# Kernel tuning notes

Hardware: AMD Instinct MI355X
Metric: run time of the kernel (lower is better)

The kernel has to match this reference:

```python
import math
import jax, jax.numpy as jnp
import numpy as np

D, H, L, DFF, V = 512, 8, 6, 2048, 32000
B, S = 2, 2048
PAD = 1


def _layernorm(x, g, b, eps=1e-5):
    m = x.mean(-1, keepdims=True)
    v = ((x - m) ** 2).mean(-1, keepdims=True)
    return (x - m) / jnp.sqrt(v + eps) * g + b


def _mha(qx, kx, w, b, mask, h=H):
    # w: [4, D, D] (q,k,v,out), b: [4, D]; mask broadcastable to [B,1,Sq,Sk]
    bs, sq, d = qx.shape
    dk = d // h
    def proj(x, i):
        return (x @ w[i] + b[i]).reshape(bs, -1, h, dk).transpose(0, 2, 1, 3)
    q, k, v = proj(qx, 0), proj(kx, 1), proj(kx, 2)
    scores = jnp.einsum('bhqd,bhkd->bhqk', q, k) / math.sqrt(dk)
    scores = jnp.where(mask, scores, -jnp.inf)
    attn = jax.nn.softmax(scores, axis=-1)
    out = jnp.einsum('bhqk,bhkd->bhqd', attn, v).transpose(0, 2, 1, 3).reshape(bs, sq, d)
    return out @ w[3] + b[3]


def _ff(x, w1, b1, w2, b2):
    return jax.nn.relu(x @ w1 + b1) @ w2 + b2


def _sinusoidal_pe(max_len, d):
    pos = np.arange(max_len)[:, None].astype(np.float64)
    div = np.exp(np.arange(0, d, 2) * (-math.log(10000.0) / d))
    pe = np.zeros((max_len, d), np.float32)
    pe[:, 0::2] = np.sin(pos * div)
    pe[:, 1::2] = np.cos(pos * div)
    return jnp.asarray(pe[None])  # [1, max_len, d]


def setup_inputs() -> dict:
    key = jax.random.key(0)
    ks = iter(jax.random.split(key, 32))
    def w(shape):
        return jax.random.normal(next(ks), shape, jnp.float32) * 0.02
    inp = {
        'src': jax.random.randint(next(ks), (B, S), 2, V),
        'tgt': jax.random.randint(next(ks), (B, S), 2, V),
        'src_emb': w((V, D)),
        'tgt_emb': w((V, D)),
        'pe': _sinusoidal_pe(S, D),
        'enc_attn_w': w((L, 4, D, D)), 'enc_attn_b': jnp.zeros((L, 4, D)),
        'enc_ff_w1': w((L, D, DFF)), 'enc_ff_b1': jnp.zeros((L, DFF)),
        'enc_ff_w2': w((L, DFF, D)), 'enc_ff_b2': jnp.zeros((L, D)),
        'enc_ln_g': jnp.ones((L, 2, D)), 'enc_ln_b': jnp.zeros((L, 2, D)),
        'dec_self_w': w((L, 4, D, D)), 'dec_self_b': jnp.zeros((L, 4, D)),
        'dec_src_w': w((L, 4, D, D)), 'dec_src_b': jnp.zeros((L, 4, D)),
        'dec_ff_w1': w((L, D, DFF)), 'dec_ff_b1': jnp.zeros((L, DFF)),
        'dec_ff_w2': w((L, DFF, D)), 'dec_ff_b2': jnp.zeros((L, D)),
        'dec_ln_g': jnp.ones((L, 3, D)), 'dec_ln_b': jnp.zeros((L, 3, D)),
        'ln_g': jnp.ones((D,)), 'ln_b': jnp.zeros((D,)),
        'fc_w': w((D, V)), 'fc_b': jnp.zeros((V,)),
    }
    return inp


def reference(src, tgt, src_emb, tgt_emb, pe,
              enc_attn_w, enc_attn_b, enc_ff_w1, enc_ff_b1, enc_ff_w2, enc_ff_b2,
              enc_ln_g, enc_ln_b,
              dec_self_w, dec_self_b, dec_src_w, dec_src_b,
              dec_ff_w1, dec_ff_b1, dec_ff_w2, dec_ff_b2, dec_ln_g, dec_ln_b,
              ln_g, ln_b, fc_w, fc_b):
    s_len, t_len = src.shape[1], tgt.shape[1]
    src_mask = (src != PAD)[:, None, None, :]                      # [B,1,1,Ss]
    tril = jnp.tril(jnp.ones((t_len, t_len), bool))
    tgt_mask = (tgt != PAD)[:, None, None, :] & tril[None, None]   # [B,1,St,St]

    x = src_emb[src] + pe[:, :s_len]
    for l in range(L):
        x2 = _layernorm(x, enc_ln_g[l, 0], enc_ln_b[l, 0])
        x = x + _mha(x2, x2, enc_attn_w[l], enc_attn_b[l], src_mask)
        x2 = _layernorm(x, enc_ln_g[l, 1], enc_ln_b[l, 1])
        x = x + _ff(x2, enc_ff_w1[l], enc_ff_b1[l], enc_ff_w2[l], enc_ff_b2[l])
    memory = x

    y = tgt_emb[tgt] + pe[:, :t_len]
    for l in range(L):
        y2 = _layernorm(y, dec_ln_g[l, 0], dec_ln_b[l, 0])
        y = y + _mha(y2, y2, dec_self_w[l], dec_self_b[l], tgt_mask)
        y2 = _layernorm(y, dec_ln_g[l, 1], dec_ln_b[l, 1])
        y = y + _mha(y2, memory, dec_src_w[l], dec_src_b[l], src_mask)
        y2 = _layernorm(y, dec_ln_g[l, 2], dec_ln_b[l, 2])
        y = y + _ff(y2, dec_ff_w1[l], dec_ff_b1[l], dec_ff_w2[l], dec_ff_b2[l])

    return _layernorm(y, ln_g, ln_b) @ fc_w + fc_b  # [B, St, V]
```

## Files before the change

### kernel.cpp

```cpp
#include <hip/hip_runtime.h>
#include <math.h>

#define D_MODEL 512
#define NHEAD   8
#define NLAYER  6
#define DFF_    2048
#define VOCAB   32000
#define BATCH   2
#define SEQ     2048
#define NTOK    (BATCH*SEQ)
#define PAD_ID  1

typedef __attribute__((ext_vector_type(8))) short s16x8;
typedef __attribute__((ext_vector_type(4))) float f32x4;
typedef unsigned short u16;
typedef unsigned int   u32;
typedef unsigned long long u64;

__device__ __forceinline__ u16 f2bf(float x) {
  u32 u = __builtin_bit_cast(u32, x);
  u += 0x7FFFu + ((u >> 16) & 1u);
  return (u16)(u >> 16);
}

__device__ __forceinline__ float exp2i(float x) {
  float r; asm("v_exp_f32 %0, %1" : "=v"(r) : "v"(x)); return r;
}

__device__ __forceinline__ void gload16(const void* g, void* l) {
  __builtin_amdgcn_global_load_lds(
      (const __attribute__((address_space(1))) u32*)g,
      (__attribute__((address_space(3))) u32*)l, 16, 0, 0);
}

#define CEXP 0.1803368802f

__global__ __launch_bounds__(256) void embed2_kernel(
    const int* __restrict__ src, const int* __restrict__ tgt,
    const float* __restrict__ se, const float* __restrict__ te,
    const float* __restrict__ pe, float* __restrict__ xe, float* __restrict__ yd)
{
  const int z = blockIdx.y;
  const int* tok = z ? tgt : src;
  const float* emb = z ? te : se;
  float* out = z ? yd : xe;
  const int total = NTOK * D_MODEL;
  for (int i = blockIdx.x * 256 + threadIdx.x; i < total; i += gridDim.x * 256) {
    int t = i >> 9;
    int d = i & 511;
    int s = t & (SEQ - 1);
    out[i] = emb[(size_t)tok[t] * D_MODEL + d] + pe[(size_t)s * D_MODEL + d];
  }
}

__global__ __launch_bounds__(64) void padmask2_kernel(
    const int* __restrict__ src, const int* __restrict__ tgt,
    u64* __restrict__ pmS, u64* __restrict__ pmT)
{
  const int z = blockIdx.z;
  const int* tok = z ? tgt : src;
  u64* pm = z ? pmT : pmS;
  int b = blockIdx.y, t = blockIdx.x;
  int lane = threadIdx.x;
  u64 m = __ballot(tok[(size_t)b * SEQ + t * 64 + lane] != PAD_ID);
  if (lane == 0) pm[b * (SEQ / 64) + t] = m;
}

__global__ __launch_bounds__(256) void ln_kernel(
    const float* __restrict__ x, const float* __restrict__ g,
    const float* __restrict__ bb, u16* __restrict__ y)
{
  const int lane = threadIdx.x & 63;
  const size_t row = (size_t)blockIdx.x * 4 + (threadIdx.x >> 6);
  const float* xr = x + row * D_MODEL + lane * 8;
  float4 v0 = *(const float4*)xr;
  float4 v1 = *(const float4*)(xr + 4);
  float sum = (v0.x + v0.y) + (v0.z + v0.w) + (v1.x + v1.y) + (v1.z + v1.w);
  float ss = v0.x * v0.x + v0.y * v0.y + v0.z * v0.z + v0.w * v0.w
           + v1.x * v1.x + v1.y * v1.y + v1.z * v1.z + v1.w * v1.w;
  #pragma unroll
  for (int o = 1; o < 64; o <<= 1) {
    sum += __shfl_xor(sum, o, 64);
    ss  += __shfl_xor(ss, o, 64);
  }
  float mean = sum * (1.0f / D_MODEL);
  float inv = rsqrtf(ss * (1.0f / D_MODEL) - mean * mean + 1e-5f);
  float4 g0 = *(const float4*)&g[lane * 8];
  float4 g1 = *(const float4*)&g[lane * 8 + 4];
  float4 c0 = *(const float4*)&bb[lane * 8];
  float4 c1 = *(const float4*)&bb[lane * 8 + 4];
  uint4 o;
  o.x = (u32)f2bf((v0.x - mean) * inv * g0.x + c0.x) | ((u32)f2bf((v0.y - mean) * inv * g0.y + c0.y) << 16);
  o.y = (u32)f2bf((v0.z - mean) * inv * g0.z + c0.z) | ((u32)f2bf((v0.w - mean) * inv * g0.w + c0.w) << 16);
  o.z = (u32)f2bf((v1.x - mean) * inv * g1.x + c1.x) | ((u32)f2bf((v1.y - mean) * inv * g1.y + c1.y) << 16);
  o.w = (u32)f2bf((v1.z - mean) * inv * g1.z + c1.z) | ((u32)f2bf((v1.w - mean) * inv * g1.w + c1.w) << 16);
  *(uint4*)&y[row * D_MODEL + lane * 8] = o;
}

__global__ __launch_bounds__(256) void tconv2_kernel(
    const float* __restrict__ s0, const float* __restrict__ s1,
    u16* __restrict__ d0, u16* __restrict__ d1, int zsplit, int K, int N)
{
  __shared__ float tile[64][65];
  const int z = blockIdx.z;
  const float* src = (z < zsplit) ? s0 + (size_t)z * K * N : s1 + (size_t)(z - zsplit) * K * N;
  u16* dst = (z < zsplit) ? d0 + (size_t)z * K * N : d1 + (size_t)(z - zsplit) * K * N;
  const int n0 = blockIdx.x * 64, k0 = blockIdx.y * 64;
  const int t = threadIdx.x;
  const int cr = t >> 4, cc = (t & 15) * 4;
  #pragma unroll
  for (int it = 0; it < 4; ++it) {
    int kr = cr + it * 16;
    float4 v = *(const float4*)&src[(size_t)(k0 + kr) * N + n0 + cc];
    tile[kr][cc] = v.x; tile[kr][cc + 1] = v.y; tile[kr][cc + 2] = v.z; tile[kr][cc + 3] = v.w;
  }
  __syncthreads();
  #pragma unroll
  for (int it = 0; it < 4; ++it) {
    int nr = cr + it * 16;
    u32 lo = (u32)f2bf(tile[cc + 0][nr]) | ((u32)f2bf(tile[cc + 1][nr]) << 16);
    u32 hi = (u32)f2bf(tile[cc + 2][nr]) | ((u32)f2bf(tile[cc + 3][nr]) << 16);
    uint2 pk; pk.x = lo; pk.y = hi;
    *(uint2*)&dst[(size_t)(n0 + nr) * K + k0 + cc] = pk;
  }
}

__global__ __launch_bounds__(256) void tconv3_kernel(
    const float* __restrict__ s0, const float* __restrict__ s1,
    const float* __restrict__ s2, u16* __restrict__ dst0)
{
  __shared__ float tile[64][65];
  const int z = blockIdx.z;
  const float* src = (z < 24) ? s0 + (size_t)z * 262144
                   : (z < 48) ? s1 + (size_t)(z - 24) * 262144
                              : s2 + (size_t)(z - 48) * 262144;
  u16* dst = dst0 + (size_t)z * 262144;
  const int n0 = blockIdx.x * 64, k0 = blockIdx.y * 64;
  const int t = threadIdx.x;
  const int cr = t >> 4, cc = (t & 15) * 4;
  #pragma unroll
  for (int it = 0; it < 4; ++it) {
    int kr = cr + it * 16;
    float4 v = *(const float4*)&src[(size_t)(k0 + kr) * 512 + n0 + cc];
    tile[kr][cc] = v.x; tile[kr][cc + 1] = v.y; tile[kr][cc + 2] = v.z; tile[kr][cc + 3] = v.w;
  }
  __syncthreads();
  #pragma unroll
  for (int it = 0; it < 4; ++it) {
    int nr = cr + it * 16;
    u32 lo = (u32)f2bf(tile[cc + 0][nr]) | ((u32)f2bf(tile[cc + 1][nr]) << 16);
    u32 hi = (u32)f2bf(tile[cc + 2][nr]) | ((u32)f2bf(tile[cc + 3][nr]) << 16);
    uint2 pk; pk.x = lo; pk.y = hi;
    *(uint2*)&dst[(size_t)(n0 + nr) * 512 + k0 + cc] = pk;
  }
}

template<int MODE, int BM, int BN, int MAP>
__global__ __launch_bounds__(256, 2) void mm_kernel(
    const u16* __restrict__ A, const u16* __restrict__ Wt,
    const float* __restrict__ bias, const float* __restrict__ res,
    void* __restrict__ Cout, u16* __restrict__ vtOut,
    int M, int N, int K,
    long long wStride, long long bStride, long long cStride)
{
  constexpr int MI = BM / 32;
  constexpr int NI = BN / 32;
  constexpr bool DB = (BM == 64 && BN == 64);
  __shared__ u16 sh[(DB ? 2 : 1) * (BM + BN) * 64];
  const int z = blockIdx.z;
  size_t wOff, bOff;
  if (MAP == 1) {
    wOff = (size_t)(z >> 1) * 4 * 262144 + (size_t)(1 + (z & 1)) * 262144;
    bOff = (size_t)(z >> 1) * 4 * 512 + (size_t)(1 + (z & 1)) * 512;
  } else {
    wOff = (size_t)z * wStride;
    bOff = (size_t)z * bStride;
  }
  Wt += wOff;
  bias += bOff;
  const int bm = blockIdx.y * BM, bn = blockIdx.x * BN;
  const int tid = threadIdx.x, lane = tid & 63, w = tid >> 6;
  const int wm = w >> 1, wn = w & 1;
  const int l15 = lane & 15, l4 = lane >> 4;
  const int wrow0 = wm * (BM / 2), wcol0 = wn * (BN / 2);
  const u16* aBase = A  + (size_t)bm * K;
  const u16* bBase = Wt + (size_t)bn * K;
  f32x4 acc[MI][NI] = {};

  auto mfma_step = [&](const u16* Asb, const u16* Bsb) {
    #pragma unroll
    for (int ks = 0; ks < 2; ++ks) {
      s16x8 af[MI], bf[NI];
      #pragma unroll
      for (int mi = 0; mi < MI; ++mi) {
        int rr = wrow0 + mi * 16 + l15;
        af[mi] = *(const s16x8*)&Asb[(rr << 6) + (((ks * 4 + l4) ^ (rr & 7)) << 3)];
      }
      #pragma unroll
      for (int ni = 0; ni < NI; ++ni) {
        int rr = wcol0 + ni * 16 + l15;
        bf[ni] = *(const s16x8*)&Bsb[(rr << 6) + (((ks * 4 + l4) ^ (rr & 7)) << 3)];
      }
      #pragma unroll
      for (int mi = 0; mi < MI; ++mi)
        #pragma unroll
        for (int ni = 0; ni < NI; ++ni)
          acc[mi][ni] = __builtin_amdgcn_mfma_f32_16x16x32_bf16(af[mi], bf[ni], acc[mi][ni], 0, 0, 0);
    }
  };

  if constexpr (DB) {
    u16* As0 = sh;
    u16* As1 = sh + 64 * 64;
    u16* Bs0 = sh + 2 * 64 * 64;
    u16* Bs1 = sh + 3 * 64 * 64;
    auto stage = [&](int k0, u16* Ad, u16* Bd) {
      #pragma unroll
      for (int i = 0; i < 2; ++i) {
        int lin = i * 256 + tid;
        int r = lin >> 3, sp = lin & 7;
        gload16(aBase + (size_t)r * K + k0 + ((sp ^ (r & 7)) * 8), &Ad[(i * 256 + w * 64) * 8]);
      }
      #pragma unroll
      for (int i = 0; i < 2; ++i) {
        int lin = i * 256 + tid;
        int r = lin >> 3, sp = lin & 7;
        gload16(bBase + (size_t)r * K + k0 + ((sp ^ (r & 7)) * 8), &Bd[(i * 256 + w * 64) * 8]);
      }
    };
    stage(0, As0, Bs0);
    __syncthreads();
    const int nt = K >> 6;
    for (int t = 0; t < nt; ++t) {
      const bool even = !(t & 1);
      u16* Ac = even ? As0 : As1;
      u16* Bc = even ? Bs0 : Bs1;
      if (t + 1 < nt) stage((t + 1) << 6, even ? As1 : As0, even ? Bs1 : Bs0);
      mfma_step(Ac, Bc);
      __syncthreads();
    }
  } else {
    u16* As = sh;
    u16* Bs = sh + BM * 64;
    for (int k0 = 0; k0 < K; k0 += 64) {
      #pragma unroll
      for (int i = 0; i < BM / 32; ++i) {
        int lin = i * 256 + tid;
        int r = lin >> 3, sp = lin & 7;
        gload16(aBase + (size_t)r * K + k0 + ((sp ^ (r & 7)) * 8), &As[(i * 256 + w * 64) * 8]);
      }
      #pragma unroll
      for (int i = 0; i < BN / 32; ++i) {
        int lin = i * 256 + tid;
        int r = lin >> 3, sp = lin & 7;
        gload16(bBase + (size_t)r * K + k0 + ((sp ^ (r & 7)) * 8), &Bs[(i * 256 + w * 64) * 8]);
      }
      __syncthreads();
      mfma_step(As, Bs);
      __syncthreads();
    }
  }

  const bool vpath = (MODE == 4 && z == 2) || (MODE == 5 && (z & 1) == 1);
  if (vpath) {
    u16* TT = sh;
    #pragma unroll
    for (int mi = 0; mi < MI; ++mi)
      #pragma unroll
      for (int ni = 0; ni < NI; ++ni)
        #pragma unroll
        for (int r = 0; r < 4; ++r) {
          int rowl = wrow0 + mi * 16 + l4 * 4 + r;
          int coll = wcol0 + ni * 16 + l15;
          TT[coll * 72 + rowl] = f2bf(acc[mi][ni][r] + bias[bn + coll]);
        }
    __syncthreads();
    const int b = bm >> 11, s0loc = bm & 2047, h = bn >> 6;
    const int layer = (MODE == 5) ? (z >> 1) : 0;
    u16* vbase = vtOut + (size_t)layer * ((size_t)NTOK * D_MODEL)
               + ((size_t)(b * NHEAD + h) * 64) * SEQ;
    int d = tid >> 2, sc = (tid & 3) * 16;
    s16x8 v0 = *(const s16x8*)&TT[d * 72 + sc];
    s16x8 v1 = *(const s16x8*)&TT[d * 72 + sc + 8];
    *(s16x8*)(vbase + (size_t)d * SEQ + s0loc + sc) = v0;
    *(s16x8*)(vbase + (size_t)d * SEQ + s0loc + sc + 8) = v1;
    return;
  }

  const int zi = (MAP == 1) ? (z >> 1) : z;
  #pragma unroll
  for (int ni = 0; ni < NI; ++ni) {
    int col = bn + wcol0 + ni * 16 + l15;
    float bb = bias[col];
    #pragma unroll
    for (int mi = 0; mi < MI; ++mi) {
      #pragma unroll
      for (int r = 0; r < 4; ++r) {
        int row = bm + wrow0 + mi * 16 + l4 * 4 + r;
        size_t off = (size_t)zi * cStride + (size_t)row * N + col;
        float v = acc[mi][ni][r] + bb;
        if (MODE == 1 || MODE == 6) v += res[(size_t)row * N + col];
        if (MODE == 3) v = fmaxf(v, 0.0f);
        if (MODE <= 1 || MODE == 6) ((float*)Cout)[off] = v;
        else                        ((u16*)Cout)[off] = f2bf(v);
        if (MODE == 6) vtOut[(size_t)row * N + col] = f2bf(v);
      }
    }
  }
}

template<int CAUSAL, int QPROJ>
__global__ __launch_bounds__(256, 2) void fattn_kernel(
    const u16* __restrict__ Qg, const u16* __restrict__ Kg,
    const u16* __restrict__ Vt, const u16* __restrict__ Wq,
    const float* __restrict__ qbias, const u64* __restrict__ padm,
    u16* __restrict__ Og)
{
  __shared__ u16 Ks[2][128 * 64];
  __shared__ u16 Vs[2][64 * 128];
  __shared__ u16 Ps[4][16 * 128];
  const int qtile = CAUSAL ? (int)(gridDim.x - 1 - blockIdx.x) : (int)blockIdx.x;
  const int qt = qtile * 64;
  const int h = blockIdx.y, b = blockIdx.z;
  const int tid = threadIdx.x, lane = tid & 63, w = tid >> 6;
  const int l15 = lane & 15, l4 = lane >> 4;
  const int hoff = h * 64;
  const u16* Kbase = Kg + (size_t)(b * SEQ) * D_MODEL + hoff;
  const u16* Vbase = Vt + (size_t)(b * NHEAD + h) * 64 * SEQ;
  const u64* pmb = padm + b * (SEQ / 64);
  const int qg = qt + w * 16 + l15;

  s16x8 aq[2];
  if constexpr (QPROJ) {
    const u16* xBase = Qg + (size_t)(b * SEQ + qt) * D_MODEL;
    const u16* wBase = Wq + (size_t)hoff * D_MODEL;
    u16* Xs = Ks[0];
    u16* Wsh = Ks[0] + 64 * 64;
    f32x4 qa[4] = {};
    for (int k0 = 0; k0 < 512; k0 += 64) {
      #pragma unroll
      for (int i = 0; i < 2; ++i) {
        int lin = i * 256 + tid;
        int r = lin >> 3, sp = lin & 7;
        gload16(xBase + (size_t)r * D_MODEL + k0 + ((sp ^ (r & 7)) * 8), &Xs[(i * 256 + w * 64) * 8]);
      }
      #pragma unroll
      for (int i = 0; i < 2; ++i) {
        int lin = i * 256 + tid;
        int r = lin >> 3, sp = lin & 7;
        gload16(wBase + (size_t)r * D_MODEL + k0 + ((sp ^ (r & 7)) * 8), &Wsh[(i * 256 + w * 64) * 8]);
      }
      __syncthreads();
      #pragma unroll
      for (int ks = 0; ks < 2; ++ks) {
        int rr = w * 16 + l15;
        s16x8 xa = *(const s16x8*)&Xs[(rr << 6) + (((ks * 4 + l4) ^ (rr & 7)) << 3)];
        #pragma unroll
        for (int ni = 0; ni < 4; ++ni) {
          int rw = ni * 16 + l15;
          s16x8 wb = *(const s16x8*)&Wsh[(rw << 6) + (((ks * 4 + l4) ^ (rw & 7)) << 3)];
          qa[ni] = __builtin_amdgcn_mfma_f32_16x16x32_bf16(xa, wb, qa[ni], 0, 0, 0);
        }
      }
      __syncthreads();
    }
    u16* Qsh = (u16*)Ps;
    #pragma unroll
    for (int ni = 0; ni < 4; ++ni) {
      int col = ni * 16 + l15;
      float bb = qbias[hoff + col];
      #pragma unroll
      for (int r = 0; r < 4; ++r) {
        int row = w * 16 + l4 * 4 + r;
        Qsh[(row << 6) + ((((col >> 3)) ^ (row & 7)) << 3) + (col & 7)] = f2bf(qa[ni][r] + bb);
      }
    }
    __syncthreads();
    {
      int rr = w * 16 + l15;
      aq[0] = *(const s16x8*)&Qsh[(rr << 6) + (((0 + l4) ^ (rr & 7)) << 3)];
      aq[1] = *(const s16x8*)&Qsh[(rr << 6) + (((4 + l4) ^ (rr & 7)) << 3)];
    }
  } else {
    const u16* qp = Qg + (size_t)(b * SEQ + qg) * D_MODEL + hoff + l4 * 8;
    aq[0] = *(const s16x8*)qp;
    aq[1] = *(const s16x8*)(qp + 32);
  }

  f32x4 oacc[4] = {};
  float mrow = -1e30f, lrow = 0.f;
  const int nt = CAUSAL ? (qt >> 7) + 1 : SEQ / 128;

  #define STAGE(KV0, BUF)                                                              \
    {                                                                                  \
      _Pragma("unroll")                                                                \
      for (int it = 0; it < 4; ++it) {                                                 \
        int lin = it * 256 + tid;                                                      \
        int rr = lin >> 3, sp = lin & 7;                                               \
        gload16(Kbase + (size_t)((KV0) + rr) * D_MODEL + ((sp ^ (rr & 7)) * 8),        \
                &Ks[BUF][(it * 256 + w * 64) * 8]);                                    \
      }                                                                                \
      _Pragma("unroll")                                                                \
      for (int it = 0; it < 4; ++it) {                                                 \
        int lin = it * 256 + tid;                                                      \
        int rr = lin >> 4, ko = lin & 15;                                              \
        gload16(Vbase + (size_t)rr * SEQ + (KV0) + ((ko ^ (rr & 15)) * 8),             \
                &Vs[BUF][(it * 256 + w * 64) * 8]);                                    \
      }                                                                                \
    }

  if constexpr (QPROJ) __syncthreads();
  STAGE(0, 0);
  __syncthreads();

  for (int kt = 0; kt < nt; ++kt) {
    const int kv0 = kt * 128;
    const int cur = kt & 1;
    if (kt + 1 < nt) STAGE(kv0 + 128, cur ^ 1);

    f32x4 sac[8] = {};
    #pragma unroll
    for (int ks = 0; ks < 2; ++ks)
      #pragma unroll
      for (int jn = 0; jn < 8; ++jn) {
        int rr = jn * 16 + l15;
        s16x8 ak = *(const s16x8*)&Ks[cur][(rr << 6) + (((ks * 4 + l4) ^ (rr & 7)) << 3)];
        sac[jn] = __builtin_amdgcn_mfma_f32_16x16x32_bf16(ak, aq[ks], sac[jn], 0, 0, 0);
      }

    const u64 m0 = pmb[(kv0 >> 6)];
    const u64 m1 = pmb[(kv0 >> 6) + 1];
    const bool lastC = CAUSAL && (kt == nt - 1);
    if (((m0 & m1) != ~0ull) || lastC) {
      #pragma unroll
      for (int jn = 0; jn < 8; ++jn) {
        u64 mm = (jn < 4) ? m0 : m1;
        #pragma unroll
        for (int r = 0; r < 4; ++r) {
          int kl = (jn & 3) * 16 + l4 * 4 + r;
          int kvg = kv0 + jn * 16 + l4 * 4 + r;
          bool ok = ((mm >> kl) & 1) && (!CAUSAL || kvg <= qg);
          if (!ok) sac[jn][r] = -1e30f;
        }
      }
    }

    float m = sac[0][0];
    #pragma unroll
    for (int jn = 0; jn < 8; ++jn)
      #pragma unroll
      for (int r = 0; r < 4; ++r) m = fmaxf(m, sac[jn][r]);
    m = fmaxf(m, __shfl_xor(m, 16, 64));
    m = fmaxf(m, __shfl_xor(m, 32, 64));

    if (__any(m - mrow > 64.0f)) {
      float mn = fmaxf(mrow, m);
      float sc = exp2i((mrow - mn) * CEXP);
      mrow = mn;
      lrow *= sc;
      #pragma unroll
      for (int jn = 0; jn < 4; ++jn)
        #pragma unroll
        for (int r = 0; r < 4; ++r) oacc[jn][r] *= sc;
    }

    float rs = 0.f;
    #pragma unroll
    for (int jn = 0; jn < 8; ++jn) {
      float p0 = exp2i((sac[jn][0] - mrow) * CEXP);
      float p1 = exp2i((sac[jn][1] - mrow) * CEXP);
      float p2 = exp2i((sac[jn][2] - mrow) * CEXP);
      float p3 = exp2i((sac[jn][3] - mrow) * CEXP);
      rs += (p0 + p1) + (p2 + p3);
      uint2 pk;
      pk.x = (u32)f2bf(p0) | ((u32)f2bf(p1) << 16);
      pk.y = (u32)f2bf(p2) | ((u32)f2bf(p3) << 16);
      int pu = (jn * 4 + l4) ^ ((l15 & 7) << 2);
      *(uint2*)&Ps[w][l15 * 128 + pu * 4] = pk;
    }
    rs += __shfl_xor(rs, 16, 64);
    rs += __shfl_xor(rs, 32, 64);
    lrow += rs;

    #pragma unroll
    for (int ks2 = 0; ks2 < 4; ++ks2) {
      int pu = (ks2 * 8 + l4 * 2) ^ ((l15 & 7) << 2);
      s16x8 pb = *(const s16x8*)&Ps[w][l15 * 128 + pu * 4];
      #pragma unroll
      for (int jn = 0; jn < 4; ++jn) {
        int rr = jn * 16 + l15;
        s16x8 av = *(const s16x8*)&Vs[cur][(rr << 7) + (((ks2 * 4 + l4) ^ (rr & 15)) << 3)];
        oacc[jn] = __builtin_amdgcn_mfma_f32_16x16x32_bf16(av, pb, oacc[jn], 0, 0, 0);
      }
    }
    __syncthreads();
  }
  #undef STAGE

  const float inv = 1.0f / lrow;
  u16* orow = Og + (size_t)(b * SEQ + qg) * D_MODEL + hoff;
  #pragma unroll
  for (int jn = 0; jn < 4; ++jn) {
    uint2 pk;
    pk.x = (u32)f2bf(oacc[jn][0] * inv) | ((u32)f2bf(oacc[jn][1] * inv) << 16);
    pk.y = (u32)f2bf(oacc[jn][2] * inv) | ((u32)f2bf(oacc[jn][3] * inv) << 16);
    *(uint2*)(orow + jn * 16 + l4 * 4) = pk;
  }
}

extern "C" void kernel_launch(void* const* d_in, const int* in_sizes, int n_in,
                              void* d_out, int out_size, void* d_ws, size_t ws_size,
                              hipStream_t stream)
{
  const int*   src        = (const int*)  d_in[0];
  const int*   tgt        = (const int*)  d_in[1];
  const float* src_emb    = (const float*)d_in[2];
  const float* tgt_emb    = (const float*)d_in[3];
  const float* pe         = (const float*)d_in[4];
  const float* enc_attn_w = (const float*)d_in[5];
  const float* enc_attn_b = (const float*)d_in[6];
  const float* enc_ff_w1  = (const float*)d_in[7];
  const float* enc_ff_b1  = (const float*)d_in[8];
  const float* enc_ff_w2  = (const float*)d_in[9];
  const float* enc_ff_b2  = (const float*)d_in[10];
  const float* enc_ln_g   = (const float*)d_in[11];
  const float* enc_ln_bb  = (const float*)d_in[12];
  const float* dec_self_w = (const float*)d_in[13];
  const float* dec_self_b = (const float*)d_in[14];
  const float* dec_src_w  = (const float*)d_in[15];
  const float* dec_src_b  = (const float*)d_in[16];
  const float* dec_ff_w1  = (const float*)d_in[17];
  const float* dec_ff_b1  = (const float*)d_in[18];
  const float* dec_ff_w2  = (const float*)d_in[19];
  const float* dec_ff_b2  = (const float*)d_in[20];
  const float* dec_ln_g   = (const float*)d_in[21];
  const float* dec_ln_bb  = (const float*)d_in[22];
  const float* fin_ln_g   = (const float*)d_in[23];
  const float* fin_ln_b   = (const float*)d_in[24];
  const float* fc_w       = (const float*)d_in[25];
  const float* fc_b       = (const float*)d_in[26];
  float* out = (float*)d_out;

  const size_t DD = (size_t)D_MODEL * D_MODEL;
  const size_t FD = (size_t)D_MODEL * DFF_;
  const size_t TD = (size_t)NTOK * D_MODEL;

  char* ob = (char*)d_out;
  size_t off = 0;
  auto alloco = [&](size_t bytes) { void* p = ob + off; off += (bytes + 255) & ~(size_t)255; return p; };
  u16* wt_enc_attn = (u16*)alloco(24 * DD * 2);
  u16* wt_dec_self = (u16*)alloco(24 * DD * 2);
  u16* wt_dec_src  = (u16*)alloco(24 * DD * 2);
  u16* wt_enc_ff1  = (u16*)alloco(6 * FD * 2);
  u16* wt_enc_ff2  = (u16*)alloco(6 * FD * 2);
  u16* wt_dec_ff1  = (u16*)alloco(6 * FD * 2);
  u16* wt_dec_ff2  = (u16*)alloco(6 * FD * 2);
  u16* qb   = (u16*)alloco(2 * TD * 2);
  u16* kb   = qb + TD;
  u16* vtb  = (u16*)alloco(TD * 2);
  u16* aob  = (u16*)alloco(TD * 2);
  u16* hbb  = (u16*)alloco((size_t)NTOK * DFF_ * 2);
  u16* memb = (u16*)alloco(TD * 2);
  u16* ckb  = (u16*)alloco(6 * TD * 2);
  u16* cvtb = (u16*)alloco(6 * TD * 2);

  char* wsb = (char*)d_ws;
  u16*   fcwt = (u16*)wsb;
  size_t wo = ((size_t)VOCAB * D_MODEL * 2 + 255) & ~(size_t)255;
  float* xe  = (float*)(wsb + wo); wo += TD * 4;
  float* yd  = (float*)(wsb + wo); wo += TD * 4;
  u16*   x2b = (u16*)(wsb + wo);   wo += TD * 2;
  u64*   pmS = (u64*)(wsb + wo);   wo += 1024;
  u64*   pmT = (u64*)(wsb + wo);

  dim3 blk(256);
  dim3 gN512(8, 64, 1), gQKV(8, 64, 3), gCKV(8, 64, 12);
  dim3 gFF1(16, 32, 1), gFC(125, 32, 1);
  dim3 gAttn(SEQ / 64, NHEAD, BATCH);
  dim3 gLN(NTOK / 4);
  const long long llDD = (long long)DD, llTD = (long long)TD;

  padmask2_kernel<<<dim3(SEQ / 64, BATCH, 2), dim3(64), 0, stream>>>(src, tgt, pmS, pmT);
  tconv3_kernel<<<dim3(8, 8, 72), blk, 0, stream>>>(enc_attn_w, dec_self_w, dec_src_w, wt_enc_attn);
  tconv2_kernel<<<dim3(32, 8, 12), blk, 0, stream>>>(enc_ff_w1, dec_ff_w1, wt_enc_ff1, wt_dec_ff1, 6, 512, 2048);
  tconv2_kernel<<<dim3(8, 32, 12), blk, 0, stream>>>(enc_ff_w2, dec_ff_w2, wt_enc_ff2, wt_dec_ff2, 6, 2048, 512);
  tconv2_kernel<<<dim3(500, 8, 1), blk, 0, stream>>>(fc_w, fc_w, fcwt, fcwt, 1, 512, VOCAB);
  embed2_kernel<<<dim3(2048, 2), blk, 0, stream>>>(src, tgt, src_emb, tgt_emb, pe, xe, yd);

  for (int l = 0; l < NLAYER; ++l) {
    ln_kernel<<<gLN, blk, 0, stream>>>(xe, enc_ln_g + (size_t)(l * 2 + 0) * D_MODEL,
                                       enc_ln_bb + (size_t)(l * 2 + 0) * D_MODEL, x2b);
    mm_kernel<4, 64, 64, 0><<<gQKV, blk, 0, stream>>>(x2b, wt_enc_attn + (size_t)l * 4 * DD,
        enc_attn_b + (size_t)l * 4 * D_MODEL, nullptr, qb, vtb, NTOK, 512, 512, llDD, D_MODEL, llTD);
    fattn_kernel<0, 0><<<gAttn, blk, 0, stream>>>(qb, kb, vtb, nullptr, nullptr, pmS, aob);
    mm_kernel<1, 64, 64, 0><<<gN512, blk, 0, stream>>>(aob, wt_enc_attn + (size_t)(l * 4 + 3) * DD,
        enc_attn_b + (size_t)(l * 4 + 3) * D_MODEL, xe, xe, nullptr, NTOK, 512, 512, 0, 0, 0);
    ln_kernel<<<gLN, blk, 0, stream>>>(xe, enc_ln_g + (size_t)(l * 2 + 1) * D_MODEL,
                                       enc_ln_bb + (size_t)(l * 2 + 1) * D_MODEL, x2b);
    mm_kernel<3, 128, 128, 0><<<gFF1, blk, 0, stream>>>(x2b, wt_enc_ff1 + (size_t)l * FD,
        enc_ff_b1 + (size_t)l * DFF_, nullptr, hbb, nullptr, NTOK, DFF_, 512, 0, 0, 0);
    if (l == NLAYER - 1)
      mm_kernel<6, 64, 64, 0><<<gN512, blk, 0, stream>>>(hbb, wt_enc_ff2 + (size_t)l * FD,
          enc_ff_b2 + (size_t)l * D_MODEL, xe, xe, memb, NTOK, 512, DFF_, 0, 0, 0);
    else
      mm_kernel<1, 64, 64, 0><<<gN512, blk, 0, stream>>>(hbb, wt_enc_ff2 + (size_t)l * FD,
          enc_ff_b2 + (size_t)l * D_MODEL, xe, xe, nullptr, NTOK, 512, DFF_, 0, 0, 0);
  }

  mm_kernel<5, 64, 64, 1><<<gCKV, blk, 0, stream>>>(memb, wt_dec_src, dec_src_b, nullptr,
      ckb, cvtb, NTOK, 512, 512, 0, 0, llTD);

  for (int l = 0; l < NLAYER; ++l) {
    const u16* Ws = wt_dec_self + (size_t)l * 4 * DD;
    const u16* Wc = wt_dec_src + (size_t)l * 4 * DD;
    const float* bs  = dec_self_b + (size_t)l * 4 * D_MODEL;
    const float* bcb = dec_src_b + (size_t)l * 4 * D_MODEL;
    ln_kernel<<<gLN, blk, 0, stream>>>(yd, dec_ln_g + (size_t)(l * 3 + 0) * D_MODEL,
                                       dec_ln_bb + (size_t)(l * 3 + 0) * D_MODEL, x2b);
    mm_kernel<4, 64, 64, 0><<<gQKV, blk, 0, stream>>>(x2b, Ws, bs, nullptr, qb, vtb,
                                                      NTOK, 512, 512, llDD, D_MODEL, llTD);
    fattn_kernel<1, 0><<<gAttn, blk, 0, stream>>>(qb, kb, vtb, nullptr, nullptr, pmT, aob);
    mm_kernel<1, 64, 64, 0><<<gN512, blk, 0, stream>>>(aob, Ws + 3 * DD, bs + 3 * D_MODEL, yd, yd,
                                                       nullptr, NTOK, 512, 512, 0, 0, 0);
    ln_kernel<<<gLN, blk, 0, stream>>>(yd, dec_ln_g + (size_t)(l * 3 + 1) * D_MODEL,
                                       dec_ln_bb + (size_t)(l * 3 + 1) * D_MODEL, x2b);
    fattn_kernel<0, 1><<<gAttn, blk, 0, stream>>>(x2b, ckb + (size_t)l * TD, cvtb + (size_t)l * TD,
                                                  Wc, bcb, pmS, aob);
    mm_kernel<1, 64, 64, 0><<<gN512, blk, 0, stream>>>(aob, Wc + 3 * DD, bcb + 3 * D_MODEL, yd, yd,
                                                       nullptr, NTOK, 512, 512, 0, 0, 0);
    ln_kernel<<<gLN, blk, 0, stream>>>(yd, dec_ln_g + (size_t)(l * 3 + 2) * D_MODEL,
                                       dec_ln_bb + (size_t)(l * 3 + 2) * D_MODEL, x2b);
    mm_kernel<3, 128, 128, 0><<<gFF1, blk, 0, stream>>>(x2b, wt_dec_ff1 + (size_t)l * FD,
        dec_ff_b1 + (size_t)l * DFF_, nullptr, hbb, nullptr, NTOK, DFF_, 512, 0, 0, 0);
    mm_kernel<1, 64, 64, 0><<<gN512, blk, 0, stream>>>(hbb, wt_dec_ff2 + (size_t)l * FD,
        dec_ff_b2 + (size_t)l * D_MODEL, yd, yd, nullptr, NTOK, 512, DFF_, 0, 0, 0);
  }

  ln_kernel<<<gLN, blk, 0, stream>>>(yd, fin_ln_g, fin_ln_b, x2b);
  mm_kernel<0, 128, 256, 0><<<gFC, blk, 0, stream>>>(x2b, fcwt, fc_b, nullptr, out, nullptr,
                                                     NTOK, VOCAB, 512, 0, 0, 0);

  (void)in_sizes; (void)n_in; (void)out_size; (void)ws_size;
}
```

Measured before the change: 2.285 ms.

## Shrink attention KV tile to 64, double-buffer square GEMM tiles, swap FC grid order

The flash-attention kernel now processes 64-key tiles instead of 128. This cuts shared memory and register use so launch bounds can ask for 4 blocks per SM, at the cost of twice as many loop iterations and barriers. The GEMM kernel's double-buffered path now covers any square tile size, so the 128x128 FF1 GEMM gets double buffering, which doubles its shared memory. The vocab projection grid is transposed so consecutive blocks walk the M dimension and share the same weight tile, aiming for better L2 reuse of the weights.

```diff
diff --git a/kernel.cpp b/kernel.cpp
--- a/kernel.cpp
+++ b/kernel.cpp
@@ -155,7 +155,7 @@
   }
 }
 
-template<int MODE, int BM, int BN, int MAP>
+template<int MODE, int BM, int BN, int MAP, int XSWAP = 0>
 __global__ __launch_bounds__(256, 2) void mm_kernel(
     const u16* __restrict__ A, const u16* __restrict__ Wt,
     const float* __restrict__ bias, const float* __restrict__ res,
@@ -165,7 +165,7 @@
 {
   constexpr int MI = BM / 32;
   constexpr int NI = BN / 32;
-  constexpr bool DB = (BM == 64 && BN == 64);
+  constexpr bool DB = (BM == BN);
   __shared__ u16 sh[(DB ? 2 : 1) * (BM + BN) * 64];
   const int z = blockIdx.z;
   size_t wOff, bOff;
@@ -178,7 +178,8 @@
   }
   Wt += wOff;
   bias += bOff;
-  const int bm = blockIdx.y * BM, bn = blockIdx.x * BN;
+  const int bm = (XSWAP ? blockIdx.x : blockIdx.y) * BM;
+  const int bn = (XSWAP ? blockIdx.y : blockIdx.x) * BN;
   const int tid = threadIdx.x, lane = tid & 63, w = tid >> 6;
   const int wm = w >> 1, wn = w & 1;
   const int l15 = lane & 15, l4 = lane >> 4;
@@ -211,18 +212,18 @@
 
   if constexpr (DB) {
     u16* As0 = sh;
-    u16* As1 = sh + 64 * 64;
-    u16* Bs0 = sh + 2 * 64 * 64;
-    u16* Bs1 = sh + 3 * 64 * 64;
+    u16* As1 = sh + BM * 64;
+    u16* Bs0 = sh + 2 * BM * 64;
+    u16* Bs1 = sh + 2 * BM * 64 + BN * 64;
     auto stage = [&](int k0, u16* Ad, u16* Bd) {
       #pragma unroll
-      for (int i = 0; i < 2; ++i) {
+      for (int i = 0; i < BM / 32; ++i) {
         int lin = i * 256 + tid;
         int r = lin >> 3, sp = lin & 7;
         gload16(aBase + (size_t)r * K + k0 + ((sp ^ (r & 7)) * 8), &Ad[(i * 256 + w * 64) * 8]);
       }
       #pragma unroll
-      for (int i = 0; i < 2; ++i) {
+      for (int i = 0; i < BN / 32; ++i) {
         int lin = i * 256 + tid;
         int r = lin >> 3, sp = lin & 7;
         gload16(bBase + (size_t)r * K + k0 + ((sp ^ (r & 7)) * 8), &Bd[(i * 256 + w * 64) * 8]);
@@ -310,15 +311,15 @@
 }
 
 template<int CAUSAL, int QPROJ>
-__global__ __launch_bounds__(256, 2) void fattn_kernel(
+__global__ __launch_bounds__(256, 4) void fattn_kernel(
     const u16* __restrict__ Qg, const u16* __restrict__ Kg,
     const u16* __restrict__ Vt, const u16* __restrict__ Wq,
     const float* __restrict__ qbias, const u64* __restrict__ padm,
     u16* __restrict__ Og)
 {
-  __shared__ u16 Ks[2][128 * 64];
-  __shared__ u16 Vs[2][64 * 128];
-  __shared__ u16 Ps[4][16 * 128];
+  __shared__ u16 Ks[2][64 * 64];
+  __shared__ u16 Vs[2][64 * 64];
+  __shared__ u16 Ps[4][16 * 64];
   const int qtile = CAUSAL ? (int)(gridDim.x - 1 - blockIdx.x) : (int)blockIdx.x;
   const int qt = qtile * 64;
   const int h = blockIdx.y, b = blockIdx.z;
@@ -334,8 +335,8 @@
   if constexpr (QPROJ) {
     const u16* xBase = Qg + (size_t)(b * SEQ + qt) * D_MODEL;
     const u16* wBase = Wq + (size_t)hoff * D_MODEL;
-    u16* Xs = Ks[0];
-    u16* Wsh = Ks[0] + 64 * 64;
+    u16* Xs  = Ks[0];
+    u16* Wsh = Vs[0];
     f32x4 qa[4] = {};
     for (int k0 = 0; k0 < 512; k0 += 64) {
       #pragma unroll
@@ -389,22 +390,22 @@
 
   f32x4 oacc[4] = {};
   float mrow = -1e30f, lrow = 0.f;
-  const int nt = CAUSAL ? (qt >> 7) + 1 : SEQ / 128;
+  const int nt = CAUSAL ? (qt >> 6) + 1 : SEQ / 64;
 
   #define STAGE(KV0, BUF)                                                              \
     {                                                                                  \
       _Pragma("unroll")                                                                \
-      for (int it = 0; it < 4; ++it) {                                                 \
+      for (int it = 0; it < 2; ++it) {                                                 \
         int lin = it * 256 + tid;                                                      \
         int rr = lin >> 3, sp = lin & 7;                                               \
         gload16(Kbase + (size_t)((KV0) + rr) * D_MODEL + ((sp ^ (rr & 7)) * 8),        \
                 &Ks[BUF][(it * 256 + w * 64) * 8]);                                    \
       }                                                                                \
       _Pragma("unroll")                                                                \
-      for (int it = 0; it < 4; ++it) {                                                 \
+      for (int it = 0; it < 2; ++it) {                                                 \
         int lin = it * 256 + tid;                                                      \
-        int rr = lin >> 4, ko = lin & 15;                                              \
-        gload16(Vbase + (size_t)rr * SEQ + (KV0) + ((ko ^ (rr & 15)) * 8),             \
+        int rr = lin >> 3, ko = lin & 7;                                               \
+        gload16(Vbase + (size_t)rr * SEQ + (KV0) + ((ko ^ (rr & 7)) * 8),              \
                 &Vs[BUF][(it * 256 + w * 64) * 8]);                                    \
       }                                                                                \
     }
@@ -414,32 +415,30 @@
   __syncthreads();
 
   for (int kt = 0; kt < nt; ++kt) {
-    const int kv0 = kt * 128;
+    const int kv0 = kt * 64;
     const int cur = kt & 1;
-    if (kt + 1 < nt) STAGE(kv0 + 128, cur ^ 1);
-
-    f32x4 sac[8] = {};
+    if (kt + 1 < nt) STAGE(kv0 + 64, cur ^ 1);
+
+    f32x4 sac[4] = {};
     #pragma unroll
     for (int ks = 0; ks < 2; ++ks)
       #pragma unroll
-      for (int jn = 0; jn < 8; ++jn) {
+      for (int jn = 0; jn < 4; ++jn) {
         int rr = jn * 16 + l15;
         s16x8 ak = *(const s16x8*)&Ks[cur][(rr << 6) + (((ks * 4 + l4) ^ (rr & 7)) << 3)];
         sac[jn] = __builtin_amdgcn_mfma_f32_16x16x32_bf16(ak, aq[ks], sac[jn], 0, 0, 0);
       }
 
-    const u64 m0 = pmb[(kv0 >> 6)];
-    const u64 m1 = pmb[(kv0 >> 6) + 1];
+    const u64 m0 = pmb[kv0 >> 6];
     const bool lastC = CAUSAL && (kt == nt - 1);
-    if (((m0 & m1) != ~0ull) || lastC) {
-      #pragma unroll
-      for (int jn = 0; jn < 8; ++jn) {
-        u64 mm = (jn < 4) ? m0 : m1;
+    if ((m0 != ~0ull) || lastC) {
+      #pragma unroll
+      for (int jn = 0; jn < 4; ++jn) {
         #pragma unroll
         for (int r = 0; r < 4; ++r) {
-          int kl = (jn & 3) * 16 + l4 * 4 + r;
-          int kvg = kv0 + jn * 16 + l4 * 4 + r;
-          bool ok = ((mm >> kl) & 1) && (!CAUSAL || kvg <= qg);
+          int kl = jn * 16 + l4 * 4 + r;
+          int kvg = kv0 + kl;
+          bool ok = ((m0 >> kl) & 1) && (!CAUSAL || kvg <= qg);
           if (!ok) sac[jn][r] = -1e30f;
         }
       }
@@ -447,7 +446,7 @@
 
     float m = sac[0][0];
     #pragma unroll
-    for (int jn = 0; jn < 8; ++jn)
+    for (int jn = 0; jn < 4; ++jn)
       #pragma unroll
       for (int r = 0; r < 4; ++r) m = fmaxf(m, sac[jn][r]);
     m = fmaxf(m, __shfl_xor(m, 16, 64));
@@ -466,7 +465,7 @@
 
     float rs = 0.f;
     #pragma unroll
-    for (int jn = 0; jn < 8; ++jn) {
+    for (int jn = 0; jn < 4; ++jn) {
       float p0 = exp2i((sac[jn][0] - mrow) * CEXP);
       float p1 = exp2i((sac[jn][1] - mrow) * CEXP);
       float p2 = exp2i((sac[jn][2] - mrow) * CEXP);
@@ -475,21 +474,21 @@
       uint2 pk;
       pk.x = (u32)f2bf(p0) | ((u32)f2bf(p1) << 16);
       pk.y = (u32)f2bf(p2) | ((u32)f2bf(p3) << 16);
-      int pu = (jn * 4 + l4) ^ ((l15 & 7) << 2);
-      *(uint2*)&Ps[w][l15 * 128 + pu * 4] = pk;
+      int u = (jn * 4 + l4) ^ ((l15 & 7) << 1);
+      *(uint2*)&Ps[w][l15 * 64 + u * 4] = pk;
     }
     rs += __shfl_xor(rs, 16, 64);
     rs += __shfl_xor(rs, 32, 64);
     lrow += rs;
 
     #pragma unroll
-    for (int ks2 = 0; ks2 < 4; ++ks2) {
-      int pu = (ks2 * 8 + l4 * 2) ^ ((l15 & 7) << 2);
-      s16x8 pb = *(const s16x8*)&Ps[w][l15 * 128 + pu * 4];
+    for (int ks2 = 0; ks2 < 2; ++ks2) {
+      int up = (ks2 * 8 + l4 * 2) ^ ((l15 & 7) << 1);
+      s16x8 pb = *(const s16x8*)&Ps[w][l15 * 64 + up * 4];
       #pragma unroll
       for (int jn = 0; jn < 4; ++jn) {
         int rr = jn * 16 + l15;
-        s16x8 av = *(const s16x8*)&Vs[cur][(rr << 7) + (((ks2 * 4 + l4) ^ (rr & 15)) << 3)];
+        s16x8 av = *(const s16x8*)&Vs[cur][(rr << 6) + (((ks2 * 4 + l4) ^ (rr & 7)) << 3)];
         oacc[jn] = __builtin_amdgcn_mfma_f32_16x16x32_bf16(av, pb, oacc[jn], 0, 0, 0);
       }
     }
@@ -575,7 +574,7 @@
 
   dim3 blk(256);
   dim3 gN512(8, 64, 1), gQKV(8, 64, 3), gCKV(8, 64, 12);
-  dim3 gFF1(16, 32, 1), gFC(125, 32, 1);
+  dim3 gFF1(16, 32, 1), gFC(32, 125, 1);
   dim3 gAttn(SEQ / 64, NHEAD, BATCH);
   dim3 gLN(NTOK / 4);
   const long long llDD = (long long)DD, llTD = (long long)TD;
@@ -637,8 +636,8 @@
   }
 
   ln_kernel<<<gLN, blk, 0, stream>>>(yd, fin_ln_g, fin_ln_b, x2b);
-  mm_kernel<0, 128, 256, 0><<<gFC, blk, 0, stream>>>(x2b, fcwt, fc_b, nullptr, out, nullptr,
-                                                     NTOK, VOCAB, 512, 0, 0, 0);
+  mm_kernel<0, 128, 256, 0, 1><<<gFC, blk, 0, stream>>>(x2b, fcwt, fc_b, nullptr, out, nullptr,
+                                                        NTOK, VOCAB, 512, 0, 0, 0);
 
   (void)in_sizes; (void)n_in; (void)out_size; (void)ws_size;
 }
```

New measurement: 2.340 ms. 1.02x slower.
